# Kernel optimization log

Hardware: AMD Instinct MI355X
Metric: run time of the kernel (lower is better)

Reference implementation:

```python
import jax, jax.numpy as jnp
import numpy as np

D_MODEL = 768
HIDDEN = 2048  # round(768*8/3)=2048, already a multiple of 64
N_EXPERTS = 8
ALPHA = 0.05  # load_balance_alpha


def setup_inputs() -> dict:
    key = jax.random.key(0)
    k0, k1, k2, k3, k4 = jax.random.split(key, 5)
    x = jax.random.normal(k0, (2, 2048, D_MODEL), dtype=jnp.float32)
    wg_w = jax.random.normal(k1, (N_EXPERTS, D_MODEL), dtype=jnp.float32) * 0.02
    wg_b = jnp.zeros((N_EXPERTS,), dtype=jnp.float32)
    Wu = jax.random.normal(k2, (N_EXPERTS, D_MODEL, HIDDEN), dtype=jnp.float32) * 0.02
    Wv = jax.random.normal(k3, (N_EXPERTS, D_MODEL, HIDDEN), dtype=jnp.float32) * 0.02
    Wd = jax.random.normal(k4, (N_EXPERTS, HIDDEN, D_MODEL), dtype=jnp.float32) * 0.02
    return {"x": x, "wg_w": wg_w, "wg_b": wg_b, "Wu": Wu, "Wv": Wv, "Wd": Wd}


def reference(x, wg_w, wg_b, Wu, Wv, Wd):
    b, t, d = x.shape
    xf = x.reshape(b * t, d)  # [N, d]

    # ---- Top1Router (eval mode: temp=1, no noise, z_loss_coef=0) ----
    logits = xf @ wg_w.T + wg_b            # [N, E]
    probs = jax.nn.softmax(logits, axis=-1)
    top1_idx = jnp.argmax(logits, axis=-1)  # [N]
    top1_p = jnp.take_along_axis(probs, top1_idx[:, None], axis=1)[:, 0]  # [N]

    # aux loss: me and ce computed under no_grad in the torch source -> stop_gradient
    one_hot = jax.nn.one_hot(top1_idx, N_EXPERTS, dtype=probs.dtype)
    me = jax.lax.stop_gradient(one_hot.mean(axis=0))   # [E]
    ce = jax.lax.stop_gradient(probs.mean(axis=0))     # [E]
    aux = ALPHA * N_EXPERTS * jnp.sum(me * ce)

    # ---- Dropless dispatch: per-expert masked SwiGLU, combined with top1 gate ----
    gate = top1_p[:, None]  # [N, 1]
    y = jnp.zeros_like(xf)
    for e in range(N_EXPERTS):
        mask = (top1_idx == e)[:, None]            # [N, 1]
        xe = jnp.where(mask, xf, 0.0)              # zero-out non-routed tokens (no biases -> exact)
        u = xe @ Wu[e]                              # [N, H]
        v = xe @ Wv[e]                              # [N, H]
        ye = (jax.nn.silu(u) * v) @ Wd[e]           # [N, d]
        y = y + jnp.where(mask, ye * gate, 0.0)
    return y.reshape(b, t, d), aux
```

## Files before the change

### kernel.cpp

```cpp
#include <hip/hip_runtime.h>
#include <cstdint>
#include <cstddef>

#define TOK 4096
#define DM 768
#define HID 2048
#define NE 8

typedef __attribute__((ext_vector_type(8))) short bf16x8;
typedef __attribute__((ext_vector_type(4))) float f32x4;

#define ASYNC16(GP, LP) \
  __builtin_amdgcn_global_load_lds((__attribute__((address_space(1))) void*)(GP), \
                                   (__attribute__((address_space(3))) void*)(LP), 16, 0, 0)

__device__ __forceinline__ unsigned short f2bf(float f) {
  unsigned int u = __float_as_uint(f);
  u += 0x7FFF + ((u >> 16) & 1);
  return (unsigned short)(u >> 16);
}
__device__ __forceinline__ unsigned int pack2(float a, float b) {
  return (unsigned)f2bf(a) | ((unsigned)f2bf(b) << 16);
}
__device__ __forceinline__ int padded_off(const int* counts, int e) {
  int o = 0;
  for (int i = 0; i < e; ++i) o += (counts[i] + 127) & ~127;
  return o;
}


__global__ __launch_bounds__(256)
void k1_gate_convert(const float* __restrict__ x, const float* __restrict__ wgw,
                     const float* __restrict__ wgb,
                     const float* __restrict__ Wu, const float* __restrict__ Wv,
                     const float* __restrict__ Wd,
                     int* __restrict__ eidx, float* __restrict__ gatep,
                     int* __restrict__ pos, int* __restrict__ counts,
                     float* __restrict__ cepart,
                     unsigned short* __restrict__ wub, unsigned short* __restrict__ wvb,
                     unsigned short* __restrict__ wdb)
{
  __shared__ float ce_loc[4][NE];
  const int b = blockIdx.x;
  if (b < 1024) {
    const int lane = threadIdx.x & 63;
    const int w = threadIdx.x >> 6;
    const int t = b * 4 + w;
    float acc[NE];
#pragma unroll
    for (int e = 0; e < NE; ++e) acc[e] = 0.f;
    const float* xr = x + (size_t)t * DM;
#pragma unroll
    for (int j = 0; j < DM / 64; ++j) {
      float xv = xr[j * 64 + lane];
#pragma unroll
      for (int e = 0; e < NE; ++e) acc[e] += xv * wgw[e * DM + j * 64 + lane];
    }
#pragma unroll
    for (int e = 0; e < NE; ++e) {
      float v = acc[e];
#pragma unroll
      for (int off = 32; off >= 1; off >>= 1) v += __shfl_xor(v, off);
      acc[e] = v + wgb[e];
    }
    float mx = acc[0]; int ai = 0;
#pragma unroll
    for (int e = 1; e < NE; ++e) if (acc[e] > mx) { mx = acc[e]; ai = e; }
    float p[NE]; float se = 0.f;
#pragma unroll
    for (int e = 0; e < NE; ++e) { p[e] = expf(acc[e] - mx); se += p[e]; }
    float inv = 1.f / se;
    if (lane == 0) {
#pragma unroll
      for (int e = 0; e < NE; ++e) ce_loc[w][e] = p[e] * inv;
      eidx[t] = ai;
      gatep[t] = p[ai] * inv;
      pos[t] = atomicAdd(&counts[ai], 1);
    }
    __syncthreads();
    if (threadIdx.x < NE) {
      float s = ce_loc[0][threadIdx.x] + ce_loc[1][threadIdx.x]
              + ce_loc[2][threadIdx.x] + ce_loc[3][threadIdx.x];
      cepart[b * NE + threadIdx.x] = s;
    }
    return;
  }
  const int cb = b - 1024;
  const int seg = cb / 3072;
  const int r = cb % 3072;
  const int e = r / 384;
  const int rem = r % 384;
  const float* W;
  unsigned short* blob;
  int N, nt, kt;
  if (seg < 2) {
    N = HID; nt = rem / 24; kt = rem % 24;
    W = (seg == 0) ? Wu : Wv;
    blob = ((seg == 0) ? wub : wvb) + (size_t)((e * 16 + nt) * 24 + kt) * 4096;
    W += (size_t)e * DM * HID;
  } else {
    N = DM; nt = rem / 64; kt = rem % 64;
    W = Wd + (size_t)e * HID * DM;
    blob = wdb + (size_t)((e * 6 + nt) * 64 + kt) * 4096;
  }
  const int t = threadIdx.x;
#pragma unroll
  for (int c = 0; c < 2; ++c) {
    const int unit = c * 256 + t;
    const int nl = unit >> 2, s = unit & 3, ko = s ^ (nl & 3);
    const float* src = W + (size_t)(kt * 32 + ko * 8) * N + nt * 128 + nl;
    uint4 u;
    u.x = pack2(src[0], src[(size_t)N]);
    u.y = pack2(src[(size_t)2 * N], src[(size_t)3 * N]);
    u.z = pack2(src[(size_t)4 * N], src[(size_t)5 * N]);
    u.w = pack2(src[(size_t)6 * N], src[(size_t)7 * N]);
    *(uint4*)(blob + (size_t)unit * 8) = u;
  }
}

__global__ __launch_bounds__(256)
void k2_scatter_zero_aux(const float* __restrict__ x, const int* __restrict__ eidx,
                         const float* __restrict__ gatep, const int* __restrict__ pos,
                         const int* __restrict__ counts, const float* __restrict__ cepart,
                         int* __restrict__ tlist, float* __restrict__ gate_b,
                         unsigned short* __restrict__ xb,
                         float* __restrict__ y, float* __restrict__ aux_out)
{
  __shared__ float sl[256][NE];
  const int b = blockIdx.x;
  if (b < 1024) {
    const int lane = threadIdx.x & 63;
    const int w = threadIdx.x >> 6;
    const int t = b * 4 + w;
    const int e = eidx[t];
    const int prow = padded_off(counts, e) + pos[t];
    if (lane == 0) { tlist[prow] = t; gate_b[prow] = gatep[t]; }
    const int tile = prow >> 7, m = prow & 127;
    const float* xr = x + (size_t)t * DM;
#pragma unroll
    for (int c = 0; c < 2; ++c) {
      int u = c * 64 + lane;
      if (u < 96) {
        int kt = u >> 2, ko = u & 3;
        const float4* s4 = (const float4*)(xr + kt * 32 + ko * 8);
        float4 v0 = s4[0], v1 = s4[1];
        uint4 d;
        d.x = pack2(v0.x, v0.y); d.y = pack2(v0.z, v0.w);
        d.z = pack2(v1.x, v1.y); d.w = pack2(v1.z, v1.w);
        int slot = m * 4 + (ko ^ (m & 3));
        *(uint4*)(xb + ((size_t)(tile * 24 + kt) * 512 + slot) * 8) = d;
      }
    }
  } else if (b < 1536) {
    float4* y4 = (float4*)y;
    const int base = (b - 1024) * 1536 + threadIdx.x;
#pragma unroll
    for (int c = 0; c < 6; ++c) {
      float4 z; z.x = 0.f; z.y = 0.f; z.z = 0.f; z.w = 0.f;
      y4[base + c * 256] = z;
    }
  } else {
    const int tid = threadIdx.x;
    float s[NE];
#pragma unroll
    for (int e = 0; e < NE; ++e) s[e] = 0.f;
    for (int bb = tid; bb < 1024; bb += 256)
#pragma unroll
      for (int e = 0; e < NE; ++e) s[e] += cepart[bb * NE + e];
#pragma unroll
    for (int e = 0; e < NE; ++e) sl[tid][e] = s[e];
    __syncthreads();
    for (int st = 128; st > 0; st >>= 1) {
      if (tid < st)
#pragma unroll
        for (int e = 0; e < NE; ++e) sl[tid][e] += sl[tid + st][e];
      __syncthreads();
    }
    if (tid == 0) {
      float aux = 0.f;
      for (int e = 0; e < NE; ++e)
        aux += ((float)counts[e] / 4096.f) * (sl[0][e] / 4096.f);
      aux_out[0] = 0.05f * 8.f * aux;
    }
  }
}

__global__ __launch_bounds__(256, 2)
void k_ffn1(const unsigned short* __restrict__ wub, const unsigned short* __restrict__ wvb,
            const unsigned short* __restrict__ xb, const float* __restrict__ gate_b,
            const int* __restrict__ counts, unsigned short* __restrict__ h)
{
  const int e = blockIdx.z;
  const int Me = counts[e];
  const int tm = blockIdx.y;
  if (tm * 128 >= Me) return;
  const int tn = blockIdx.x;
  const int prowbase = padded_off(counts, e) + tm * 128;
  const int atile = prowbase >> 7;

  __shared__ __align__(16) unsigned short Sh[12288];

  const int tid = threadIdx.x;
  const int lane = tid & 63;
  const int wv_ = tid >> 6;
  const int wm = wv_ >> 1, wn = wv_ & 1;
  const int wu_id = __builtin_amdgcn_readfirstlane(wv_);

  f32x4 accU[4][4], accV[4][4];
#pragma unroll
  for (int i = 0; i < 4; ++i)
#pragma unroll
    for (int j = 0; j < 4; ++j)
#pragma unroll
      for (int k = 0; k < 4; ++k) { accU[i][j][k] = 0.f; accV[i][j][k] = 0.f; }

  const char* AbBase = (const char*)xb + ((size_t)(atile * 24) << 13);
  const char* BuBase = (const char*)wub + ((size_t)((e * 16 + tn) * 24) << 13);
  const char* BvBase = (const char*)wvb + ((size_t)((e * 16 + tn) * 24) << 13);
  const int lc = lane & 15, q = lane >> 4;

  for (int kt = 0; kt < 24; ++kt) {
    const char* Ab = AbBase + ((size_t)kt << 13);
    const char* Bub = BuBase + ((size_t)kt << 13);
    const char* Bvb = BvBase + ((size_t)kt << 13);
#pragma unroll
    for (int c2 = 0; c2 < 6; ++c2) {
      const int c = wu_id * 6 + c2;
      const char* g;
      if (c < 8)       g = Ab + c * 1024 + lane * 16;
      else if (c < 16) g = Bub + (c - 8) * 1024 + lane * 16;
      else             g = Bvb + (c - 16) * 1024 + lane * 16;
      ASYNC16(g, (char*)Sh + (unsigned)(c * 1024));
    }
    __syncthreads();
    bf16x8 a[4], bu[4], bv[4];
#pragma unroll
    for (int i = 0; i < 4; ++i) {
      int m = wm * 64 + i * 16 + lc;
      a[i] = *(const bf16x8*)&Sh[(m * 4 + (q ^ (m & 3))) * 8];
    }
#pragma unroll
    for (int j = 0; j < 4; ++j) {
      int n = wn * 64 + j * 16 + lc;
      int slb = (n * 4 + (q ^ (n & 3))) * 8;
      bu[j] = *(const bf16x8*)&Sh[4096 + slb];
      bv[j] = *(const bf16x8*)&Sh[8192 + slb];
    }
#pragma unroll
    for (int i = 0; i < 4; ++i)
#pragma unroll
      for (int j = 0; j < 4; ++j) {
        accU[i][j] = __builtin_amdgcn_mfma_f32_16x16x32_bf16(a[i], bu[j], accU[i][j], 0, 0, 0);
        accV[i][j] = __builtin_amdgcn_mfma_f32_16x16x32_bf16(a[i], bv[j], accV[i][j], 0, 0, 0);
      }
    __syncthreads();
  }
  const int colbase = tn * 128 + wn * 64;
  const int rlane = (lane >> 4) * 4;
  const int clane = lane & 15;
#pragma unroll
  for (int i = 0; i < 4; ++i) {
#pragma unroll
    for (int r = 0; r < 4; ++r) {
      int rowIn = wm * 64 + i * 16 + rlane + r;
      if (tm * 128 + rowIn < Me) {
        int prow = prowbase + rowIn;
        float g = gate_b[prow];
        unsigned short* hp = h + (size_t)prow * HID + colbase + clane;
#pragma unroll
        for (int j = 0; j < 4; ++j) {
          float u_ = accU[i][j][r];
          float v_ = accV[i][j][r];
          float sv = u_ / (1.f + expf(-u_));
          hp[j * 16] = f2bf(sv * v_ * g);
        }
      }
    }
  }
}

__global__ __launch_bounds__(256, 2)
void k_ffn2(const unsigned short* __restrict__ wdb, const unsigned short* __restrict__ h,
            const int* __restrict__ counts, const int* __restrict__ tlist,
            float* __restrict__ y)
{
  const int z = blockIdx.z;
  const int e = z >> 2, split = z & 3;
  const int Me = counts[e];
  const int tm = blockIdx.y;
  if (tm * 128 >= Me) return;
  const int tn = blockIdx.x;
  const int prowbase = padded_off(counts, e) + tm * 128;

  __shared__ __align__(16) unsigned short Sh[8192];

  const int tid = threadIdx.x;
  const int lane = tid & 63;
  const int wv_ = tid >> 6;
  const int wm = wv_ >> 1, wn = wv_ & 1;
  const int wu_id = __builtin_amdgcn_readfirstlane(wv_);

  f32x4 acc[4][4];
#pragma unroll
  for (int i = 0; i < 4; ++i)
#pragma unroll
    for (int j = 0; j < 4; ++j)
#pragma unroll
      for (int k = 0; k < 4; ++k) acc[i][j][k] = 0.f;

  const char* hB = (const char*)h + (size_t)prowbase * (HID * 2);
  const char* BdBase = (const char*)wdb + ((size_t)((e * 6 + tn) * 64) << 13);
  const int lc = lane & 15, q = lane >> 4;

  for (int kti = 0; kti < 16; ++kti) {
    const int ktg = split * 16 + kti;
    const char* Bb = BdBase + ((size_t)ktg << 13);
#pragma unroll
    for (int c2 = 0; c2 < 4; ++c2) {
      const int c = wu_id * 4 + c2;
      const char* g;
      if (c < 8) {
        int mrow = c * 16 + (lane >> 2);
        int ko = (lane & 3) ^ (mrow & 3);
        g = hB + (size_t)mrow * (HID * 2) + ktg * 64 + ko * 16;
      } else {
        g = Bb + (c - 8) * 1024 + lane * 16;
      }
      ASYNC16(g, (char*)Sh + (unsigned)(c * 1024));
    }
    __syncthreads();
    bf16x8 a[4], bfr[4];
#pragma unroll
    for (int i = 0; i < 4; ++i) {
      int m = wm * 64 + i * 16 + lc;
      a[i] = *(const bf16x8*)&Sh[(m * 4 + (q ^ (m & 3))) * 8];
    }
#pragma unroll
    for (int j = 0; j < 4; ++j) {
      int n = wn * 64 + j * 16 + lc;
      bfr[j] = *(const bf16x8*)&Sh[4096 + (n * 4 + (q ^ (n & 3))) * 8];
    }
#pragma unroll
    for (int i = 0; i < 4; ++i)
#pragma unroll
      for (int j = 0; j < 4; ++j)
        acc[i][j] = __builtin_amdgcn_mfma_f32_16x16x32_bf16(a[i], bfr[j], acc[i][j], 0, 0, 0);
    __syncthreads();
  }
  const int colbase = tn * 128 + wn * 64;
  const int rlane = (lane >> 4) * 4;
  const int clane = lane & 15;
#pragma unroll
  for (int i = 0; i < 4; ++i) {
#pragma unroll
    for (int r = 0; r < 4; ++r) {
      int rowIn = wm * 64 + i * 16 + rlane + r;
      if (tm * 128 + rowIn < Me) {
        int tok = tlist[prowbase + rowIn];
        float* yp = y + (size_t)tok * DM + colbase + clane;
#pragma unroll
        for (int j = 0; j < 4; ++j) atomicAdd(&yp[j * 16], acc[i][j][r]);
      }
    }
  }
}

extern "C" void kernel_launch(void* const* d_in, const int* in_sizes, int n_in,
                              void* d_out, int out_size, void* d_ws, size_t ws_size,
                              hipStream_t stream)
{
  const float* x   = (const float*)d_in[0];
  const float* wgw = (const float*)d_in[1];
  const float* wgb = (const float*)d_in[2];
  const float* Wu  = (const float*)d_in[3];
  const float* Wv  = (const float*)d_in[4];
  const float* Wd  = (const float*)d_in[5];
  float* out = (float*)d_out;

  char* ws = (char*)d_ws;
  int*   counts = (int*)(ws + 0);
  int*   eidx   = (int*)(ws + 256);
  float* gatep  = (float*)(ws + 16640);
  int*   pos    = (int*)(ws + 33024);
  float* cepart = (float*)(ws + 49408);
  int*   tlist  = (int*)(ws + 82176);
  float* gate_b = (float*)(ws + 102656);
  unsigned short* xb  = (unsigned short*)(ws + 123136);
  unsigned short* h   = (unsigned short*)(ws + 7987456);
  unsigned short* wub = (unsigned short*)(ws + 28958976);
  unsigned short* wvb = (unsigned short*)(ws + 54124800);
  unsigned short* wdb = (unsigned short*)(ws + 79290624);

  hipMemsetAsync(counts, 0, 32, stream);
  k1_gate_convert<<<10240, 256, 0, stream>>>(x, wgw, wgb, Wu, Wv, Wd,
                                             eidx, gatep, pos, counts, cepart,
                                             wub, wvb, wdb);
  k2_scatter_zero_aux<<<1537, 256, 0, stream>>>(x, eidx, gatep, pos, counts, cepart,
                                                tlist, gate_b, xb,
                                                out, out + (size_t)TOK * DM);
  k_ffn1<<<dim3(16, 32, 8), 256, 0, stream>>>(wub, wvb, xb, gate_b, counts, h);
  k_ffn2<<<dim3(6, 32, 32), 256, 0, stream>>>(wdb, h, counts, tlist, out);
}
```

Baseline: 378.9 us.

## Vectorize weight conversion and store activations row-major with swizzled gather loads

The weight fp32→bf16 conversion now has each block handle two k-tiles. Each thread reads float4s along N, which coalesces the global reads and halves the grid. The token scatter now writes bf16 rows in plain row-major order. The FFN kernels gather those rows with a per-lane XOR swizzle, using pointers precomputed once and advanced by a fixed stride each k-step. This cuts per-iteration address arithmetic and uncoalesced fp32 reads, but the activation loads now touch 16-byte pieces spread across rows instead of contiguous 1KB chunks.

```diff
diff --git a/kernel.cpp b/kernel.cpp
--- a/kernel.cpp
+++ b/kernel.cpp
@@ -86,35 +86,38 @@
     return;
   }
   const int cb = b - 1024;
-  const int seg = cb / 3072;
-  const int r = cb % 3072;
-  const int e = r / 384;
-  const int rem = r % 384;
+  const int seg = cb / 1536;
+  const int r = cb % 1536;
+  const int e = r / 192;
+  const int rem = r % 192;
   const float* W;
-  unsigned short* blob;
-  int N, nt, kt;
+  unsigned short* blobbase;
+  int N, nt, kt2;
   if (seg < 2) {
-    N = HID; nt = rem / 24; kt = rem % 24;
-    W = (seg == 0) ? Wu : Wv;
-    blob = ((seg == 0) ? wub : wvb) + (size_t)((e * 16 + nt) * 24 + kt) * 4096;
-    W += (size_t)e * DM * HID;
+    N = HID; nt = rem / 12; kt2 = rem % 12;
+    W = ((seg == 0) ? Wu : Wv) + (size_t)e * DM * HID;
+    blobbase = ((seg == 0) ? wub : wvb) + ((size_t)((e * 16 + nt) * 24) << 12);
   } else {
-    N = DM; nt = rem / 64; kt = rem % 64;
+    N = DM; nt = rem / 32; kt2 = rem % 32;
     W = Wd + (size_t)e * HID * DM;
-    blob = wdb + (size_t)((e * 6 + nt) * 64 + kt) * 4096;
+    blobbase = wdb + ((size_t)((e * 6 + nt) * 64) << 12);
   }
   const int t = threadIdx.x;
-#pragma unroll
-  for (int c = 0; c < 2; ++c) {
-    const int unit = c * 256 + t;
-    const int nl = unit >> 2, s = unit & 3, ko = s ^ (nl & 3);
-    const float* src = W + (size_t)(kt * 32 + ko * 8) * N + nt * 128 + nl;
+  const int n4 = t & 31, ko8 = t >> 5;
+  const float* src = W + (size_t)(kt2 * 64 + ko8 * 8) * N + nt * 128 + n4 * 4;
+  float4 f[8];
+#pragma unroll
+  for (int j = 0; j < 8; ++j) f[j] = *(const float4*)(src + (size_t)j * N);
+  const int kt = kt2 * 2 + (ko8 >> 2), ko = ko8 & 3;
+  unsigned short* dst = blobbase + ((size_t)kt << 12) + (size_t)(ko * 128 + n4 * 4) * 8;
+#pragma unroll
+  for (int i = 0; i < 4; ++i) {
     uint4 u;
-    u.x = pack2(src[0], src[(size_t)N]);
-    u.y = pack2(src[(size_t)2 * N], src[(size_t)3 * N]);
-    u.z = pack2(src[(size_t)4 * N], src[(size_t)5 * N]);
-    u.w = pack2(src[(size_t)6 * N], src[(size_t)7 * N]);
-    *(uint4*)(blob + (size_t)unit * 8) = u;
+    u.x = pack2(((const float*)&f[0])[i], ((const float*)&f[1])[i]);
+    u.y = pack2(((const float*)&f[2])[i], ((const float*)&f[3])[i]);
+    u.z = pack2(((const float*)&f[4])[i], ((const float*)&f[5])[i]);
+    u.w = pack2(((const float*)&f[6])[i], ((const float*)&f[7])[i]);
+    *(uint4*)(dst + i * 8) = u;
   }
 }
 
@@ -135,21 +138,13 @@
     const int e = eidx[t];
     const int prow = padded_off(counts, e) + pos[t];
     if (lane == 0) { tlist[prow] = t; gate_b[prow] = gatep[t]; }
-    const int tile = prow >> 7, m = prow & 127;
-    const float* xr = x + (size_t)t * DM;
-#pragma unroll
-    for (int c = 0; c < 2; ++c) {
-      int u = c * 64 + lane;
-      if (u < 96) {
-        int kt = u >> 2, ko = u & 3;
-        const float4* s4 = (const float4*)(xr + kt * 32 + ko * 8);
-        float4 v0 = s4[0], v1 = s4[1];
-        uint4 d;
-        d.x = pack2(v0.x, v0.y); d.y = pack2(v0.z, v0.w);
-        d.z = pack2(v1.x, v1.y); d.w = pack2(v1.z, v1.w);
-        int slot = m * 4 + (ko ^ (m & 3));
-        *(uint4*)(xb + ((size_t)(tile * 24 + kt) * 512 + slot) * 8) = d;
-      }
+    const float4* src4 = (const float4*)(x + (size_t)t * DM);
+    uint2* dst = (uint2*)(xb + (size_t)prow * DM);
+#pragma unroll
+    for (int c = 0; c < 3; ++c) {
+      float4 v = src4[lane + c * 64];
+      uint2 d; d.x = pack2(v.x, v.y); d.y = pack2(v.z, v.w);
+      dst[lane + c * 64] = d;
     }
   } else if (b < 1536) {
     float4* y4 = (float4*)y;
@@ -196,7 +191,6 @@
   if (tm * 128 >= Me) return;
   const int tn = blockIdx.x;
   const int prowbase = padded_off(counts, e) + tm * 128;
-  const int atile = prowbase >> 7;
 
   __shared__ __align__(16) unsigned short Sh[12288];
 
@@ -214,23 +208,34 @@
 #pragma unroll
       for (int k = 0; k < 4; ++k) { accU[i][j][k] = 0.f; accV[i][j][k] = 0.f; }
 
-  const char* AbBase = (const char*)xb + ((size_t)(atile * 24) << 13);
   const char* BuBase = (const char*)wub + ((size_t)((e * 16 + tn) * 24) << 13);
   const char* BvBase = (const char*)wvb + ((size_t)((e * 16 + tn) * 24) << 13);
+
+  const char* sp[6]; size_t stp[6];
+#pragma unroll
+  for (int c2 = 0; c2 < 6; ++c2) {
+    const int c = wu_id * 6 + c2;
+    if (c < 8) {
+      int s = c * 64 + lane, m = s >> 2, ko = (s & 3) ^ (m & 3);
+      sp[c2] = (const char*)xb + (size_t)(prowbase + m) * (DM * 2) + ko * 16;
+      stp[c2] = 64;
+    } else if (c < 16) {
+      int u = (c - 8) * 64 + lane, n = u >> 2, ko = (u & 3) ^ (n & 3);
+      sp[c2] = BuBase + (size_t)(ko * 128 + n) * 16;
+      stp[c2] = 8192;
+    } else {
+      int u = (c - 16) * 64 + lane, n = u >> 2, ko = (u & 3) ^ (n & 3);
+      sp[c2] = BvBase + (size_t)(ko * 128 + n) * 16;
+      stp[c2] = 8192;
+    }
+  }
   const int lc = lane & 15, q = lane >> 4;
 
   for (int kt = 0; kt < 24; ++kt) {
-    const char* Ab = AbBase + ((size_t)kt << 13);
-    const char* Bub = BuBase + ((size_t)kt << 13);
-    const char* Bvb = BvBase + ((size_t)kt << 13);
 #pragma unroll
     for (int c2 = 0; c2 < 6; ++c2) {
-      const int c = wu_id * 6 + c2;
-      const char* g;
-      if (c < 8)       g = Ab + c * 1024 + lane * 16;
-      else if (c < 16) g = Bub + (c - 8) * 1024 + lane * 16;
-      else             g = Bvb + (c - 16) * 1024 + lane * 16;
-      ASYNC16(g, (char*)Sh + (unsigned)(c * 1024));
+      ASYNC16(sp[c2], (char*)Sh + (unsigned)((wu_id * 6 + c2) * 1024));
+      sp[c2] += stp[c2];
     }
     __syncthreads();
     bf16x8 a[4], bu[4], bv[4];
@@ -308,25 +313,29 @@
 #pragma unroll
       for (int k = 0; k < 4; ++k) acc[i][j][k] = 0.f;
 
-  const char* hB = (const char*)h + (size_t)prowbase * (HID * 2);
   const char* BdBase = (const char*)wdb + ((size_t)((e * 6 + tn) * 64) << 13);
+
+  const char* sp[4]; size_t stp[4];
+#pragma unroll
+  for (int c2 = 0; c2 < 4; ++c2) {
+    const int c = wu_id * 4 + c2;
+    if (c < 8) {
+      int s = c * 64 + lane, m = s >> 2, ko = (s & 3) ^ (m & 3);
+      sp[c2] = (const char*)h + (size_t)(prowbase + m) * (HID * 2) + split * 1024 + ko * 16;
+      stp[c2] = 64;
+    } else {
+      int u = (c - 8) * 64 + lane, n = u >> 2, ko = (u & 3) ^ (n & 3);
+      sp[c2] = BdBase + (size_t)split * 131072 + (size_t)(ko * 128 + n) * 16;
+      stp[c2] = 8192;
+    }
+  }
   const int lc = lane & 15, q = lane >> 4;
 
   for (int kti = 0; kti < 16; ++kti) {
-    const int ktg = split * 16 + kti;
-    const char* Bb = BdBase + ((size_t)ktg << 13);
 #pragma unroll
     for (int c2 = 0; c2 < 4; ++c2) {
-      const int c = wu_id * 4 + c2;
-      const char* g;
-      if (c < 8) {
-        int mrow = c * 16 + (lane >> 2);
-        int ko = (lane & 3) ^ (mrow & 3);
-        g = hB + (size_t)mrow * (HID * 2) + ktg * 64 + ko * 16;
-      } else {
-        g = Bb + (c - 8) * 1024 + lane * 16;
-      }
-      ASYNC16(g, (char*)Sh + (unsigned)(c * 1024));
+      ASYNC16(sp[c2], (char*)Sh + (unsigned)((wu_id * 4 + c2) * 1024));
+      sp[c2] += stp[c2];
     }
     __syncthreads();
     bf16x8 a[4], bfr[4];
@@ -392,9 +401,9 @@
   unsigned short* wdb = (unsigned short*)(ws + 79290624);
 
   hipMemsetAsync(counts, 0, 32, stream);
-  k1_gate_convert<<<10240, 256, 0, stream>>>(x, wgw, wgb, Wu, Wv, Wd,
-                                             eidx, gatep, pos, counts, cepart,
-                                             wub, wvb, wdb);
+  k1_gate_convert<<<1024 + 4608, 256, 0, stream>>>(x, wgw, wgb, Wu, Wv, Wd,
+                                                   eidx, gatep, pos, counts, cepart,
+                                                   wub, wvb, wdb);
   k2_scatter_zero_aux<<<1537, 256, 0, stream>>>(x, eidx, gatep, pos, counts, cepart,
                                                 tlist, gate_b, xb,
                                                 out, out + (size_t)TOK * DM);
```

After: 375.9 us. About the same (-0.8%).
